# Performance work log

Measured on AMD Instinct MI355X. Metric: run time of the kernel, lower is better.

The kernel has to match this reference:

```python
import jax, jax.numpy as jnp
import numpy as np

NEG_BIG = -1.0e9


def setup_inputs() -> dict:
    key = jax.random.key(0)
    ks = jax.random.split(key, 8)
    B, N, D = 4, 384, 256
    s = 1.0 / np.sqrt(D)
    return {
        "q": jax.random.normal(ks[0], (B, N, D), dtype=jnp.float32),
        "k": jax.random.normal(ks[1], (B, N, D), dtype=jnp.float32),
        "v": jax.random.normal(ks[2], (B, N, D), dtype=jnp.float32),
        "mask": jax.random.randint(ks[3], (B, 1, N, N), 0, 2, dtype=jnp.int32),
        "Wq": jax.random.normal(ks[4], (D, D), dtype=jnp.float32) * s,
        "bq": jnp.zeros((D,), dtype=jnp.float32),
        "Wk": jax.random.normal(ks[5], (D, D), dtype=jnp.float32) * s,
        "bk": jnp.zeros((D,), dtype=jnp.float32),
        "Wv": jax.random.normal(ks[6], (D, D), dtype=jnp.float32) * s,
        "bv": jnp.zeros((D,), dtype=jnp.float32),
    }


def reference(q, k, v, mask, Wq, bq, Wk, bk, Wv, bv):
    # Dense projections
    query = q @ Wq + bq   # [B, N, D]
    key_p = k @ Wk + bk   # [B, M, D]
    value = v @ Wv + bv   # [B, M, D]
    # Per-channel outer-product scores: [B, D, N, M]
    score = jnp.einsum('bnd,bmd->bdnm', query, key_p)
    score = score + mask.astype(score.dtype) * NEG_BIG  # mask broadcasts [B,1,N,M]
    weights = jnp.tanh(score)
    # Per-channel weighted sum back to [B, N, D]
    out = jnp.einsum('bdnm,bmd->bnd', weights, value)
    return out
```

## Files before the change

kernel.cpp:

```cpp
#include <hip/hip_runtime.h>

#define DD 256
#define NN 384
#define BB 4
#define BN (BB * NN)
#define MSPLIT 4
#define MCHUNK (NN / MSPLIT)
#define PSTRIDE (BN * DD)

constexpr float TWO_LOG2E = 2.8853900817779268f;
constexpr float MASK_X    = -1.0e9f * 2.8853900817779268f;

__global__ __launch_bounds__(256) void proj_kernel(
    const float* __restrict__ q,  const float* __restrict__ k,  const float* __restrict__ v,
    const float* __restrict__ Wq, const float* __restrict__ Wk, const float* __restrict__ Wv,
    const float* __restrict__ bq, const float* __restrict__ bk, const float* __restrict__ bv,
    float* __restrict__ Qout, float* __restrict__ KVout)
{
    const int tid  = threadIdx.x;
    const int lane = tid & 63;
    const int wv   = tid >> 6;
    const int row0 = blockIdx.x * 8;
    const int which = blockIdx.y;

    const float* X; const float* W; const float* bias; float scale; float* out; int ostride;
    if (which == 0)      { X = q; W = Wq; bias = bq; scale = 1.0f;      out = Qout;      ostride = 1; }
    else if (which == 1) { X = k; W = Wk; bias = bk; scale = TWO_LOG2E; out = KVout;     ostride = 2; }
    else                 { X = v; W = Wv; bias = bv; scale = 1.0f;      out = KVout + 1; ostride = 2; }

    __shared__ float ps[4][8][DD];

    const int k0 = wv * 64;
    const float* Xb = X + (size_t)row0 * DD + k0;
    const float* Wp = W + (size_t)k0 * DD + lane * 4;

    float4 acc[8];
    #pragma unroll
    for (int r = 0; r < 8; ++r) acc[r] = make_float4(0.f, 0.f, 0.f, 0.f);

    #pragma unroll 2
    for (int g = 0; g < 16; ++g) {
        float4 xq[8];
        #pragma unroll
        for (int r = 0; r < 8; ++r)
            xq[r] = *reinterpret_cast<const float4*>(Xb + r * DD + g * 4);
        float4 wq[4];
        #pragma unroll
        for (int u = 0; u < 4; ++u)
            wq[u] = *reinterpret_cast<const float4*>(Wp + (size_t)(g * 4 + u) * DD);
        #pragma unroll
        for (int u = 0; u < 4; ++u) {
            const float4 w = wq[u];
            #pragma unroll
            for (int r = 0; r < 8; ++r) {
                const float x = (u == 0) ? xq[r].x : (u == 1) ? xq[r].y
                              : (u == 2) ? xq[r].z : xq[r].w;
                acc[r].x = fmaf(x, w.x, acc[r].x);
                acc[r].y = fmaf(x, w.y, acc[r].y);
                acc[r].z = fmaf(x, w.z, acc[r].z);
                acc[r].w = fmaf(x, w.w, acc[r].w);
            }
        }
    }

    #pragma unroll
    for (int r = 0; r < 8; ++r)
        *reinterpret_cast<float4*>(&ps[wv][r][lane * 4]) = acc[r];
    __syncthreads();

    for (int e = tid; e < 8 * DD; e += 256) {
        const int r = e >> 8;
        const int d = e & 255;
        const float s = (ps[0][r][d] + ps[1][r][d]) + (ps[2][r][d] + ps[3][r][d]);
        out[((size_t)(row0 + r) * DD + d) * ostride] = (s + bias[d]) * scale;
    }
}

__global__ __launch_bounds__(256) void mhsa_kernel(
    const float* __restrict__ Q, const float* __restrict__ KV,
    const int* __restrict__ mask, float* __restrict__ outp)
{
    const int tid = threadIdx.x;
    const int b   = blockIdx.y;
    const int n0  = blockIdx.x * 4;
    const int m0  = blockIdx.z * MCHUNK;

    __shared__ float mf[MCHUNK][4];
    for (int idx = tid; idx < MCHUNK * 4; idx += 256) {
        const int m = idx % MCHUNK;
        const int j = idx / MCHUNK;
        mf[m][j] = mask[(size_t)(b * NN + n0 + j) * NN + (m0 + m)] ? MASK_X : 0.0f;
    }
    __syncthreads();

    float qv0 = Q[(size_t)(b * NN + n0 + 0) * DD + tid];
    float qv1 = Q[(size_t)(b * NN + n0 + 1) * DD + tid];
    float qv2 = Q[(size_t)(b * NN + n0 + 2) * DD + tid];
    float qv3 = Q[(size_t)(b * NN + n0 + 3) * DD + tid];

    const float2* kvp = reinterpret_cast<const float2*>(KV)
                      + (size_t)b * NN * DD + (size_t)m0 * DD + tid;

    float acc0 = 0.f, acc1 = 0.f, acc2 = 0.f, acc3 = 0.f, vsum = 0.f;

#define COMP(KVV, MLOC)                                                       \
    {                                                                         \
        const float4 m4 = *reinterpret_cast<const float4*>(&mf[MLOC][0]);     \
        const float kk = (KVV).x, vv = (KVV).y;                               \
        const float t2 = -2.0f * vv;                                          \
        vsum += vv;                                                           \
        const float x0 = fmaf(qv0, kk, m4.x);                                 \
        const float x1 = fmaf(qv1, kk, m4.y);                                 \
        const float x2 = fmaf(qv2, kk, m4.z);                                 \
        const float x3 = fmaf(qv3, kk, m4.w);                                 \
        acc0 = fmaf(t2, __builtin_amdgcn_rcpf(__builtin_amdgcn_exp2f(x0) + 1.0f), acc0); \
        acc1 = fmaf(t2, __builtin_amdgcn_rcpf(__builtin_amdgcn_exp2f(x1) + 1.0f), acc1); \
        acc2 = fmaf(t2, __builtin_amdgcn_rcpf(__builtin_amdgcn_exp2f(x2) + 1.0f), acc2); \
        acc3 = fmaf(t2, __builtin_amdgcn_rcpf(__builtin_amdgcn_exp2f(x3) + 1.0f), acc3); \
    }

#define LOADG(B0, B1, B2, B3, M0)                \
    B0 = kvp[(size_t)((M0) + 0) * DD];           \
    B1 = kvp[(size_t)((M0) + 1) * DD];           \
    B2 = kvp[(size_t)((M0) + 2) * DD];           \
    B3 = kvp[(size_t)((M0) + 3) * DD];

    float2 A0, A1, A2, A3, B0, B1, B2, B3;
    LOADG(A0, A1, A2, A3, 0)
    LOADG(B0, B1, B2, B3, 4)

    for (int mg = 0; mg < MCHUNK; mg += 8) {
        COMP(A0, mg + 0) COMP(A1, mg + 1) COMP(A2, mg + 2) COMP(A3, mg + 3)
        LOADG(A0, A1, A2, A3, mg + 8)
        COMP(B0, mg + 4) COMP(B1, mg + 5) COMP(B2, mg + 6) COMP(B3, mg + 7)
        LOADG(B0, B1, B2, B3, mg + 12)
    }
#undef COMP
#undef LOADG

    float* po = outp + (size_t)blockIdx.z * PSTRIDE;
    po[(size_t)(b * NN + n0 + 0) * DD + tid] = acc0 + vsum;
    po[(size_t)(b * NN + n0 + 1) * DD + tid] = acc1 + vsum;
    po[(size_t)(b * NN + n0 + 2) * DD + tid] = acc2 + vsum;
    po[(size_t)(b * NN + n0 + 3) * DD + tid] = acc3 + vsum;
}

__global__ __launch_bounds__(256) void reduce4_kernel(
    const float* __restrict__ part, float* __restrict__ out)
{
    const int i = blockIdx.x * 256 + threadIdx.x;
    out[i] = (part[i] + part[i + PSTRIDE])
           + (part[i + 2 * PSTRIDE] + part[i + 3 * PSTRIDE]);
}

extern "C" void kernel_launch(void* const* d_in, const int* in_sizes, int n_in,
                              void* d_out, int out_size, void* d_ws, size_t ws_size,
                              hipStream_t stream) {
    const float* q    = (const float*)d_in[0];
    const float* k    = (const float*)d_in[1];
    const float* v    = (const float*)d_in[2];
    const int*   mask = (const int*)  d_in[3];
    const float* Wq   = (const float*)d_in[4];
    const float* bq   = (const float*)d_in[5];
    const float* Wk   = (const float*)d_in[6];
    const float* bk   = (const float*)d_in[7];
    const float* Wv   = (const float*)d_in[8];
    const float* bv   = (const float*)d_in[9];
    float* out = (float*)d_out;

    float* Qws   = (float*)d_ws;
    float* KVws  = Qws  + (size_t)BN * DD;
    float* Pws   = KVws + (size_t)2 * BN * DD;

    dim3 g1(BN / 8, 3);
    proj_kernel<<<g1, 256, 0, stream>>>(q, k, v, Wq, Wk, Wv, bq, bk, bv, Qws, KVws);

    dim3 g2(NN / 4, BB, MSPLIT);
    mhsa_kernel<<<g2, 256, 0, stream>>>(Qws, KVws, mask, Pws);

    reduce4_kernel<<<dim3(BN * DD / 256), 256, 0, stream>>>(Pws, out);
}
```

Before: 129.5 us.

## Process eight query rows per block, split M eight ways, simplify projection

```diff
diff --git a/kernel.cpp b/kernel.cpp
--- a/kernel.cpp
+++ b/kernel.cpp
@@ -4,8 +4,9 @@
 #define NN 384
 #define BB 4
 #define BN (BB * NN)
-#define MSPLIT 4
+#define MSPLIT 8
 #define MCHUNK (NN / MSPLIT)
+#define ROWS 8
 #define PSTRIDE (BN * DD)
 
 constexpr float TWO_LOG2E = 2.8853900817779268f;
@@ -20,7 +21,7 @@
     const int tid  = threadIdx.x;
     const int lane = tid & 63;
     const int wv   = tid >> 6;
-    const int row0 = blockIdx.x * 8;
+    const int row  = blockIdx.x * 8 + wv * 2;
     const int which = blockIdx.y;
 
     const float* X; const float* W; const float* bias; float scale; float* out; int ostride;
@@ -28,51 +29,59 @@
     else if (which == 1) { X = k; W = Wk; bias = bk; scale = TWO_LOG2E; out = KVout;     ostride = 2; }
     else                 { X = v; W = Wv; bias = bv; scale = 1.0f;      out = KVout + 1; ostride = 2; }
 
-    __shared__ float ps[4][8][DD];
+    const float* X0 = X + (size_t)row * DD;
+    const float* X1 = X0 + DD;
+    const float* Wp = W + lane * 4;
 
-    const int k0 = wv * 64;
-    const float* Xb = X + (size_t)row0 * DD + k0;
-    const float* Wp = W + (size_t)k0 * DD + lane * 4;
-
-    float4 acc[8];
-    #pragma unroll
-    for (int r = 0; r < 8; ++r) acc[r] = make_float4(0.f, 0.f, 0.f, 0.f);
+    float4 a0 = make_float4(0.f, 0.f, 0.f, 0.f);
+    float4 a1 = make_float4(0.f, 0.f, 0.f, 0.f);
 
     #pragma unroll 2
-    for (int g = 0; g < 16; ++g) {
-        float4 xq[8];
-        #pragma unroll
-        for (int r = 0; r < 8; ++r)
-            xq[r] = *reinterpret_cast<const float4*>(Xb + r * DD + g * 4);
-        float4 wq[4];
-        #pragma unroll
-        for (int u = 0; u < 4; ++u)
-            wq[u] = *reinterpret_cast<const float4*>(Wp + (size_t)(g * 4 + u) * DD);
-        #pragma unroll
-        for (int u = 0; u < 4; ++u) {
-            const float4 w = wq[u];
-            #pragma unroll
-            for (int r = 0; r < 8; ++r) {
-                const float x = (u == 0) ? xq[r].x : (u == 1) ? xq[r].y
-                              : (u == 2) ? xq[r].z : xq[r].w;
-                acc[r].x = fmaf(x, w.x, acc[r].x);
-                acc[r].y = fmaf(x, w.y, acc[r].y);
-                acc[r].z = fmaf(x, w.z, acc[r].z);
-                acc[r].w = fmaf(x, w.w, acc[r].w);
-            }
-        }
+    for (int kk = 0; kk < DD; kk += 4) {
+        const float4 x0 = *reinterpret_cast<const float4*>(X0 + kk);
+        const float4 x1 = *reinterpret_cast<const float4*>(X1 + kk);
+        const float4 w0 = *reinterpret_cast<const float4*>(Wp + (size_t)(kk + 0) * DD);
+        const float4 w1 = *reinterpret_cast<const float4*>(Wp + (size_t)(kk + 1) * DD);
+        const float4 w2 = *reinterpret_cast<const float4*>(Wp + (size_t)(kk + 2) * DD);
+        const float4 w3 = *reinterpret_cast<const float4*>(Wp + (size_t)(kk + 3) * DD);
+
+        a0.x = fmaf(x0.x, w0.x, a0.x); a0.y = fmaf(x0.x, w0.y, a0.y);
+        a0.z = fmaf(x0.x, w0.z, a0.z); a0.w = fmaf(x0.x, w0.w, a0.w);
+        a1.x = fmaf(x1.x, w0.x, a1.x); a1.y = fmaf(x1.x, w0.y, a1.y);
+        a1.z = fmaf(x1.x, w0.z, a1.z); a1.w = fmaf(x1.x, w0.w, a1.w);
+
+        a0.x = fmaf(x0.y, w1.x, a0.x); a0.y = fmaf(x0.y, w1.y, a0.y);
+        a0.z = fmaf(x0.y, w1.z, a0.z); a0.w = fmaf(x0.y, w1.w, a0.w);
+        a1.x = fmaf(x1.y, w1.x, a1.x); a1.y = fmaf(x1.y, w1.y, a1.y);
+        a1.z = fmaf(x1.y, w1.z, a1.z); a1.w = fmaf(x1.y, w1.w, a1.w);
+
+        a0.x = fmaf(x0.z, w2.x, a0.x); a0.y = fmaf(x0.z, w2.y, a0.y);
+        a0.z = fmaf(x0.z, w2.z, a0.z); a0.w = fmaf(x0.z, w2.w, a0.w);
+        a1.x = fmaf(x1.z, w2.x, a1.x); a1.y = fmaf(x1.z, w2.y, a1.y);
+        a1.z = fmaf(x1.z, w2.z, a1.z); a1.w = fmaf(x1.z, w2.w, a1.w);
+
+        a0.x = fmaf(x0.w, w3.x, a0.x); a0.y = fmaf(x0.w, w3.y, a0.y);
+        a0.z = fmaf(x0.w, w3.z, a0.z); a0.w = fmaf(x0.w, w3.w, a0.w);
+        a1.x = fmaf(x1.w, w3.x, a1.x); a1.y = fmaf(x1.w, w3.y, a1.y);
+        a1.z = fmaf(x1.w, w3.z, a1.z); a1.w = fmaf(x1.w, w3.w, a1.w);
     }
 
-    #pragma unroll
-    for (int r = 0; r < 8; ++r)
-        *reinterpret_cast<float4*>(&ps[wv][r][lane * 4]) = acc[r];
-    __syncthreads();
+    const float4 bb = *reinterpret_cast<const float4*>(bias + lane * 4);
+    const float r0x = (a0.x + bb.x) * scale, r0y = (a0.y + bb.y) * scale;
+    const float r0z = (a0.z + bb.z) * scale, r0w = (a0.w + bb.w) * scale;
+    const float r1x = (a1.x + bb.x) * scale, r1y = (a1.y + bb.y) * scale;
+    const float r1z = (a1.z + bb.z) * scale, r1w = (a1.w + bb.w) * scale;
 
-    for (int e = tid; e < 8 * DD; e += 256) {
-        const int r = e >> 8;
-        const int d = e & 255;
-        const float s = (ps[0][r][d] + ps[1][r][d]) + (ps[2][r][d] + ps[3][r][d]);
-        out[((size_t)(row0 + r) * DD + d) * ostride] = (s + bias[d]) * scale;
+    if (ostride == 1) {
+        *reinterpret_cast<float4*>(out + (size_t)row * DD + lane * 4)
+            = make_float4(r0x, r0y, r0z, r0w);
+        *reinterpret_cast<float4*>(out + (size_t)(row + 1) * DD + lane * 4)
+            = make_float4(r1x, r1y, r1z, r1w);
+    } else {
+        float* o0 = out + ((size_t)row * DD + lane * 4) * 2;
+        float* o1 = out + ((size_t)(row + 1) * DD + lane * 4) * 2;
+        o0[0] = r0x; o0[2] = r0y; o0[4] = r0z; o0[6] = r0w;
+        o1[0] = r1x; o1[2] = r1y; o1[4] = r1z; o1[6] = r1w;
     }
 }
 
@@ -82,41 +91,45 @@
 {
     const int tid = threadIdx.x;
     const int b   = blockIdx.y;
-    const int n0  = blockIdx.x * 4;
+    const int n0  = blockIdx.x * ROWS;
     const int m0  = blockIdx.z * MCHUNK;
 
-    __shared__ float mf[MCHUNK][4];
-    for (int idx = tid; idx < MCHUNK * 4; idx += 256) {
+    __shared__ float mf[MCHUNK][ROWS];
+    for (int idx = tid; idx < MCHUNK * ROWS; idx += 256) {
         const int m = idx % MCHUNK;
         const int j = idx / MCHUNK;
         mf[m][j] = mask[(size_t)(b * NN + n0 + j) * NN + (m0 + m)] ? MASK_X : 0.0f;
     }
     __syncthreads();
 
-    float qv0 = Q[(size_t)(b * NN + n0 + 0) * DD + tid];
-    float qv1 = Q[(size_t)(b * NN + n0 + 1) * DD + tid];
-    float qv2 = Q[(size_t)(b * NN + n0 + 2) * DD + tid];
-    float qv3 = Q[(size_t)(b * NN + n0 + 3) * DD + tid];
+    const float* Qp = Q + (size_t)(b * NN + n0) * DD + tid;
+    float qv0 = Qp[0 * DD], qv1 = Qp[1 * DD], qv2 = Qp[2 * DD], qv3 = Qp[3 * DD];
+    float qv4 = Qp[4 * DD], qv5 = Qp[5 * DD], qv6 = Qp[6 * DD], qv7 = Qp[7 * DD];
 
     const float2* kvp = reinterpret_cast<const float2*>(KV)
                       + (size_t)b * NN * DD + (size_t)m0 * DD + tid;
 
-    float acc0 = 0.f, acc1 = 0.f, acc2 = 0.f, acc3 = 0.f, vsum = 0.f;
+    float acc0 = 0.f, acc1 = 0.f, acc2 = 0.f, acc3 = 0.f;
+    float acc4 = 0.f, acc5 = 0.f, acc6 = 0.f, acc7 = 0.f, vsum = 0.f;
 
-#define COMP(KVV, MLOC)                                                       \
-    {                                                                         \
-        const float4 m4 = *reinterpret_cast<const float4*>(&mf[MLOC][0]);     \
-        const float kk = (KVV).x, vv = (KVV).y;                               \
-        const float t2 = -2.0f * vv;                                          \
-        vsum += vv;                                                           \
-        const float x0 = fmaf(qv0, kk, m4.x);                                 \
-        const float x1 = fmaf(qv1, kk, m4.y);                                 \
-        const float x2 = fmaf(qv2, kk, m4.z);                                 \
-        const float x3 = fmaf(qv3, kk, m4.w);                                 \
-        acc0 = fmaf(t2, __builtin_amdgcn_rcpf(__builtin_amdgcn_exp2f(x0) + 1.0f), acc0); \
-        acc1 = fmaf(t2, __builtin_amdgcn_rcpf(__builtin_amdgcn_exp2f(x1) + 1.0f), acc1); \
-        acc2 = fmaf(t2, __builtin_amdgcn_rcpf(__builtin_amdgcn_exp2f(x2) + 1.0f), acc2); \
-        acc3 = fmaf(t2, __builtin_amdgcn_rcpf(__builtin_amdgcn_exp2f(x3) + 1.0f), acc3); \
+#define TANH1(ACC, XV, T2) \
+    ACC = fmaf(T2, __builtin_amdgcn_rcpf(__builtin_amdgcn_exp2f(XV) + 1.0f), ACC);
+
+#define COMP(KVV, MLOC)                                                        \
+    {                                                                          \
+        const float4 ma = *reinterpret_cast<const float4*>(&mf[MLOC][0]);      \
+        const float4 mb = *reinterpret_cast<const float4*>(&mf[MLOC][4]);      \
+        const float kk = (KVV).x, vv = (KVV).y;                                \
+        const float t2 = -2.0f * vv;                                           \
+        vsum += vv;                                                            \
+        TANH1(acc0, fmaf(qv0, kk, ma.x), t2)                                   \
+        TANH1(acc1, fmaf(qv1, kk, ma.y), t2)                                   \
+        TANH1(acc2, fmaf(qv2, kk, ma.z), t2)                                   \
+        TANH1(acc3, fmaf(qv3, kk, ma.w), t2)                                   \
+        TANH1(acc4, fmaf(qv4, kk, mb.x), t2)                                   \
+        TANH1(acc5, fmaf(qv5, kk, mb.y), t2)                                   \
+        TANH1(acc6, fmaf(qv6, kk, mb.z), t2)                                   \
+        TANH1(acc7, fmaf(qv7, kk, mb.w), t2)                                   \
     }
 
 #define LOADG(B0, B1, B2, B3, M0)                \
@@ -136,21 +149,25 @@
         LOADG(B0, B1, B2, B3, mg + 12)
     }
 #undef COMP
+#undef TANH1
 #undef LOADG
 
-    float* po = outp + (size_t)blockIdx.z * PSTRIDE;
-    po[(size_t)(b * NN + n0 + 0) * DD + tid] = acc0 + vsum;
-    po[(size_t)(b * NN + n0 + 1) * DD + tid] = acc1 + vsum;
-    po[(size_t)(b * NN + n0 + 2) * DD + tid] = acc2 + vsum;
-    po[(size_t)(b * NN + n0 + 3) * DD + tid] = acc3 + vsum;
+    float* po = outp + (size_t)blockIdx.z * PSTRIDE + (size_t)(b * NN + n0) * DD + tid;
+    po[0 * DD] = acc0 + vsum; po[1 * DD] = acc1 + vsum;
+    po[2 * DD] = acc2 + vsum; po[3 * DD] = acc3 + vsum;
+    po[4 * DD] = acc4 + vsum; po[5 * DD] = acc5 + vsum;
+    po[6 * DD] = acc6 + vsum; po[7 * DD] = acc7 + vsum;
 }
 
-__global__ __launch_bounds__(256) void reduce4_kernel(
+__global__ __launch_bounds__(256) void reduce8_kernel(
     const float* __restrict__ part, float* __restrict__ out)
 {
     const int i = blockIdx.x * 256 + threadIdx.x;
-    out[i] = (part[i] + part[i + PSTRIDE])
-           + (part[i + 2 * PSTRIDE] + part[i + 3 * PSTRIDE]);
+    float s0 = part[i + 0 * PSTRIDE] + part[i + 1 * PSTRIDE];
+    float s1 = part[i + 2 * PSTRIDE] + part[i + 3 * PSTRIDE];
+    float s2 = part[i + 4 * PSTRIDE] + part[i + 5 * PSTRIDE];
+    float s3 = part[i + 6 * PSTRIDE] + part[i + 7 * PSTRIDE];
+    out[i] = (s0 + s1) + (s2 + s3);
 }
 
 extern "C" void kernel_launch(void* const* d_in, const int* in_sizes, int n_in,
@@ -175,8 +192,8 @@
     dim3 g1(BN / 8, 3);
     proj_kernel<<<g1, 256, 0, stream>>>(q, k, v, Wq, Wk, Wv, bq, bk, bv, Qws, KVws);
 
-    dim3 g2(NN / 4, BB, MSPLIT);
+    dim3 g2(NN / ROWS, BB, MSPLIT);
     mhsa_kernel<<<g2, 256, 0, stream>>>(Qws, KVws, mask, Pws);
 
-    reduce4_kernel<<<dim3(BN * DD / 256), 256, 0, stream>>>(Pws, out);
+    reduce8_kernel<<<dim3(BN * DD / 256), 256, 0, stream>>>(Pws, out);
 }
```

Measured after the change: 146.7 us. 1.13x slower.
